# Performance work log

Hardware: AMD Instinct MI355X
Metric: run time of the kernel (lower is better)

The kernel has to match this reference:

```python
import jax, jax.numpy as jnp
import numpy as np

N_EMBED = 8192
EMBED_DIM = 32
BETA = 0.25
EPS_NORM = 1e-12   # torch F.normalize eps
EPS_ENT = 1e-4     # get_entropy eps


def _l2norm(x):
    n = jnp.linalg.norm(x, axis=-1, keepdims=True)
    return x / jnp.maximum(n, EPS_NORM)


def setup_inputs() -> dict:
    key = jax.random.key(0)
    k1, k2 = jax.random.split(key)
    z = jax.random.normal(k1, (32, EMBED_DIM, 32, 32), dtype=jnp.float32)
    # embedding.weight.data.uniform_(-1/n_embed, 1/n_embed)
    embedding = jax.random.uniform(k2, (N_EMBED, EMBED_DIM), dtype=jnp.float32,
                                   minval=-1.0 / N_EMBED, maxval=1.0 / N_EMBED)
    return {"z": z, "embedding": embedding}


def reference(z, embedding):
    batch = z.shape[0]
    # bchw -> bhwc
    zt = jnp.transpose(z, (0, 2, 3, 1))
    # l2_norm branch: cosine distance via negative inner product
    zn = _l2norm(zt)
    z_flat = zn.reshape(-1, EMBED_DIM)            # [N, D], N = B*H*W
    ew = _l2norm(embedding)                       # [K, D]
    d = -jnp.matmul(z_flat, ew.T)                 # [N, K] distance matrix
    idx = jnp.argmin(jax.lax.stop_gradient(d), axis=1)  # [N]
    # codebook usage histogram + entropy
    cb_usage = jax.ops.segment_sum(jnp.ones_like(idx, dtype=jnp.float32), idx,
                                   num_segments=N_EMBED)
    probs = (cb_usage + EPS_ENT) / jnp.sum(cb_usage + EPS_ENT)
    cb_entropy = -jnp.sum(probs * jnp.log(probs))
    # gather + re-normalize (faithful to embedding lookup then F.normalize)
    z_q = _l2norm(embedding[idx]).reshape(zn.shape)
    sg = jax.lax.stop_gradient
    loss = (BETA * jnp.mean(jnp.sum((sg(z_q) - zn) ** 2, axis=-1))
            + jnp.mean(jnp.sum((z_q - sg(zn)) ** 2, axis=-1)))
    # straight-through estimator
    z_q_st = zn + sg(z_q - zn)
    z_q_out = jnp.transpose(z_q_st, (0, 3, 1, 2))  # bhwc -> bchw
    return z_q_out, loss, cb_entropy, idx.reshape(batch, -1)
```

## Files before the change

kernel.cpp:

```cpp
#include <hip/hip_runtime.h>
#include <math.h>

#define N_EMBED 8192
#define DIM 32
#define NQ 32768

#define QPB 512
#define NQG (NQ / QPB)
#define KSPL 16
#define KCHUNK (N_EMBED / KSPL)
#define TILE 128
#define NTILES (KCHUNK / TILE)
#define NPLANE 8
#define LSTRIDE 130

#define LOSS_OFF  1048576
#define ENT_OFF   1048577
#define IDX_OFF   1048578

typedef __attribute__((ext_vector_type(8))) _Float16 half8;
typedef __attribute__((ext_vector_type(4))) float floatx4;

__global__ __launch_bounds__(512, 4) void score_kernel(const float* __restrict__ z,
                                                       const float* __restrict__ e,
                                                       unsigned long long* __restrict__ keys16,
                                                       unsigned* __restrict__ usage,
                                                       float* __restrict__ loss_acc,
                                                       unsigned* __restrict__ done_ctr) {
    __shared__ half8 lds[2][NPLANE * LSTRIDE];

    const int t = threadIdx.x;

    if (blockIdx.x == 0) {
        for (int i = t; i < N_EMBED; i += 512) usage[i] = 0u;
        if (t == 0) { loss_acc[0] = 0.f; done_ctr[0] = 0u; }
    }

    const int lane = t & 63;
    const int w = t >> 6;
    const int quad = lane >> 4;
    const int lc = lane & 15;
    const int qg = blockIdx.x & (NQG - 1);
    const int kc = blockIdx.x >> 6;
    const int kbase = kc * KCHUNK;
    const int qbase = qg * QPB + w * 64;

    half8 ah[4], am[4];
#pragma unroll
    for (int qt = 0; qt < 4; ++qt) {
        int q = qbase + qt * 16 + lc;
        const float* zp = z + (q >> 10) * (DIM * 1024) + (q & 1023);
        float x[8];
        float ss = 0.f;
#pragma unroll
        for (int j = 0; j < 8; ++j) {
            x[j] = zp[(quad * 8 + j) * 1024];
            ss = fmaf(x[j], x[j], ss);
        }
        ss += __shfl_xor(ss, 16, 64);
        ss += __shfl_xor(ss, 32, 64);
        float inv = 1.f / fmaxf(sqrtf(ss), 1e-12f);
#pragma unroll
        for (int j = 0; j < 8; ++j) {
            float xx = x[j] * inv;
            _Float16 h = (_Float16)xx;
            _Float16 m = (_Float16)((xx - (float)h) * 4096.0f);
            ah[qt][j] = h; am[qt][j] = m;
        }
    }

    auto stage = [&](int bsel, int kt) {
        const int ci = t >> 2;
        const int part = t & 3;
        const int code = kbase + kt * TILE + ci;
        const float4* er = (const float4*)(e + code * DIM) + part * 2;
        float4 v0 = er[0], v1 = er[1];
        float x[8] = {v0.x, v0.y, v0.z, v0.w, v1.x, v1.y, v1.z, v1.w};
        float ss = 0.f;
#pragma unroll
        for (int j = 0; j < 8; ++j) ss = fmaf(x[j], x[j], ss);
        ss += __shfl_xor(ss, 1, 64);
        ss += __shfl_xor(ss, 2, 64);
        float inv = 1.f / fmaxf(sqrtf(ss), 1e-12f);
        half8 h8, m8;
#pragma unroll
        for (int j = 0; j < 8; ++j) {
            float xx = x[j] * inv;
            _Float16 h = (_Float16)xx;
            _Float16 m = (_Float16)((xx - (float)h) * 4096.0f);
            h8[j] = h; m8[j] = m;
        }
        lds[bsel][part * LSTRIDE + ci] = h8;
        lds[bsel][(4 + part) * LSTRIDE + ci] = m8;
    };

    float best[16];
    int bk[16];
#pragma unroll
    for (int i = 0; i < 16; ++i) { best[i] = -2.0f; bk[i] = 0; }

    const floatx4 z4 = {0.f, 0.f, 0.f, 0.f};

    stage(0, 0);
    __syncthreads();

    for (int kt = 0; kt < NTILES; ++kt) {
        if (kt + 1 < NTILES) stage((kt + 1) & 1, kt + 1);

        const half8* __restrict__ buf = lds[kt & 1];
#pragma unroll 2
        for (int ct = 0; ct < TILE / 16; ++ct) {
            half8 bh = buf[(0 * 4 + quad) * LSTRIDE + ct * 16 + lc];
            half8 bm = buf[(1 * 4 + quad) * LSTRIDE + ct * 16 + lc];
            const int kk = kbase + kt * TILE + ct * 16 + lc;
#pragma unroll
            for (int qt = 0; qt < 4; ++qt) {
                floatx4 a0 = __builtin_amdgcn_mfma_f32_16x16x32_f16(ah[qt], bh, z4, 0, 0, 0);
                floatx4 a1 = __builtin_amdgcn_mfma_f32_16x16x32_f16(ah[qt], bm, z4, 0, 0, 0);
                a1 = __builtin_amdgcn_mfma_f32_16x16x32_f16(am[qt], bh, a1, 0, 0, 0);
#pragma unroll
                for (int r = 0; r < 4; ++r) {
                    float d = fmaf(a1[r], 0x1p-12f, a0[r]);
                    if (d > best[qt * 4 + r]) { best[qt * 4 + r] = d; bk[qt * 4 + r] = kk; }
                }
            }
        }
        __syncthreads();
    }

#pragma unroll
    for (int i = 0; i < 16; ++i) {
        unsigned ub = __float_as_uint(best[i]);
        ub = (ub & 0x80000000u) ? ~ub : (ub | 0x80000000u);
        unsigned long long key = ((unsigned long long)ub << 32) | (unsigned)(~bk[i]);
#pragma unroll
        for (int msk = 1; msk <= 8; msk <<= 1) {
            unsigned long long o = __shfl_xor(key, msk, 64);
            key = (o > key) ? o : key;
        }
        if (lc == 0) {
            int qt = i >> 2, r = i & 3;
            int q = qbase + qt * 16 + quad * 4 + r;
            keys16[kc * NQ + q] = key;
        }
    }
}

__global__ __launch_bounds__(256) void finalize_kernel(const float* __restrict__ z,
                                                       const float* __restrict__ e,
                                                       const unsigned long long* __restrict__ keys16,
                                                       unsigned* __restrict__ usage,
                                                       float* __restrict__ loss_acc,
                                                       unsigned* __restrict__ done_ctr,
                                                       float* __restrict__ out) {
    int n = blockIdx.x * 256 + threadIdx.x;
    int b  = n >> 10;
    int hw = n & 1023;
    const float* zb = z + b * (DIM * 1024) + hw;

    float q[DIM];
    float ss = 0.f;
#pragma unroll
    for (int d = 0; d < DIM; ++d) {
        q[d] = zb[d * 1024];
        ss = fmaf(q[d], q[d], ss);
    }
    float inv = 1.f / fmaxf(sqrtf(ss), 1e-12f);
#pragma unroll
    for (int d = 0; d < DIM; ++d) q[d] *= inv;

    unsigned long long bestkey = 0ull;
#pragma unroll
    for (int c = 0; c < KSPL; ++c) {
        unsigned long long k16 = keys16[c * NQ + n];
        bestkey = (k16 > bestkey) ? k16 : bestkey;
    }
    int idx = (int)(~(unsigned)(bestkey & 0xFFFFFFFFull));

    atomicAdd(&usage[idx], 1u);

    float wv[DIM];
    float ss2 = 0.f;
    const float4* er = (const float4*)(e + idx * DIM);
#pragma unroll
    for (int d8 = 0; d8 < 8; ++d8) {
        float4 t4 = er[d8];
        wv[d8*4+0] = t4.x; wv[d8*4+1] = t4.y; wv[d8*4+2] = t4.z; wv[d8*4+3] = t4.w;
        ss2 += t4.x*t4.x + t4.y*t4.y + t4.z*t4.z + t4.w*t4.w;
    }
    float inv2 = 1.f / fmaxf(sqrtf(ss2), 1e-12f);

    float lsum = 0.f;
    float* outb = out + b * (DIM * 1024) + hw;
#pragma unroll
    for (int d = 0; d < DIM; ++d) {
        float zq = wv[d] * inv2;
        float diff = zq - q[d];
        lsum = fmaf(diff, diff, lsum);
        outb[d * 1024] = q[d] + (zq - q[d]);
    }
    out[IDX_OFF + n] = (float)idx;

#pragma unroll
    for (int off = 32; off > 0; off >>= 1)
        lsum += __shfl_down(lsum, off, 64);
    if ((threadIdx.x & 63) == 0)
        atomicAdd(loss_acc, lsum);

    __shared__ unsigned lastflag;
    __syncthreads();
    if (threadIdx.x == 0) {
        __threadfence();
        unsigned prev = __hip_atomic_fetch_add(done_ctr, 1u, __ATOMIC_ACQ_REL,
                                               __HIP_MEMORY_SCOPE_AGENT);
        lastflag = (prev == gridDim.x - 1) ? 1u : 0u;
    }
    __syncthreads();
    if (lastflag) {
        __shared__ double sm[256];
        int t = threadIdx.x;
        double local = 0.0;
        const float denom = 32768.8192f;
        for (int k = t; k < N_EMBED; k += 256) {
            unsigned c = __hip_atomic_load(&usage[k], __ATOMIC_RELAXED,
                                           __HIP_MEMORY_SCOPE_AGENT);
            float p = ((float)c + 1e-4f) / denom;
            local += (double)(-(p * logf(p)));
        }
        sm[t] = local;
        __syncthreads();
        for (int s = 128; s > 0; s >>= 1) {
            if (t < s) sm[t] += sm[t + s];
            __syncthreads();
        }
        if (t == 0) {
            float la = __hip_atomic_load(loss_acc, __ATOMIC_RELAXED,
                                         __HIP_MEMORY_SCOPE_AGENT);
            out[LOSS_OFF] = (float)(1.25 * (double)la / 32768.0);
            out[ENT_OFF]  = (float)sm[0];
        }
    }
}

extern "C" void kernel_launch(void* const* d_in, const int* in_sizes, int n_in,
                              void* d_out, int out_size, void* d_ws, size_t ws_size,
                              hipStream_t stream) {
    const float* z   = (const float*)d_in[0];
    const float* emb = (const float*)d_in[1];
    float* out = (float*)d_out;

    char* ws = (char*)d_ws;
    unsigned long long* keys16 = (unsigned long long*)ws;
    unsigned* usage            = (unsigned*)(ws + (4 << 20));
    float* loss_acc            = (float*)(ws + (4 << 20) + 32768);
    unsigned* done_ctr         = (unsigned*)(ws + (4 << 20) + 32768 + 4);

    score_kernel<<<NQG * KSPL, 512, 0, stream>>>(z, emb, keys16, usage,
                                                 loss_acc, done_ctr);
    finalize_kernel<<<NQ / 256, 256, 0, stream>>>(z, emb, keys16, usage,
                                                  loss_acc, done_ctr, out);
}
```

Baseline: 144.4 us.

## Precompute split-fp16 normalized codebook in prep kernel, load whole chunk to LDS

Adds a prep kernel that normalizes the codebook once and writes fp16 hi/lo split planes to workspace. The old scheme renormalized each code in all 64 query-group blocks. The score kernel now copies its entire 512-code chunk (64KB) into LDS up front and runs the MFMA loop with no per-tile barriers or double buffering. In exchange it adds a kernel launch and a full-chunk LDS footprint, which drops occupancy to 2 blocks per CU, and it drops the LDS padding stride, which may cause bank conflicts.

```diff
diff --git a/kernel.cpp b/kernel.cpp
--- a/kernel.cpp
+++ b/kernel.cpp
@@ -9,10 +9,7 @@
 #define NQG (NQ / QPB)
 #define KSPL 16
 #define KCHUNK (N_EMBED / KSPL)
-#define TILE 128
-#define NTILES (KCHUNK / TILE)
-#define NPLANE 8
-#define LSTRIDE 130
+#define NCT (KCHUNK / 16)
 
 #define LOSS_OFF  1048576
 #define ENT_OFF   1048577
@@ -21,21 +18,46 @@
 typedef __attribute__((ext_vector_type(8))) _Float16 half8;
 typedef __attribute__((ext_vector_type(4))) float floatx4;
 
-__global__ __launch_bounds__(512, 4) void score_kernel(const float* __restrict__ z,
-                                                       const float* __restrict__ e,
-                                                       unsigned long long* __restrict__ keys16,
-                                                       unsigned* __restrict__ usage,
-                                                       float* __restrict__ loss_acc,
-                                                       unsigned* __restrict__ done_ctr) {
-    __shared__ half8 lds[2][NPLANE * LSTRIDE];
+__global__ __launch_bounds__(256) void prep_kernel(const float* __restrict__ e,
+                                                   half8* __restrict__ esplit,
+                                                   unsigned* __restrict__ usage,
+                                                   float* __restrict__ loss_acc,
+                                                   unsigned* __restrict__ done_ctr) {
+    int k = blockIdx.x * 256 + threadIdx.x;
+    const float4* src = (const float4*)(e + k * DIM);
+    float v[DIM];
+    float ss = 0.f;
+#pragma unroll
+    for (int i = 0; i < 8; ++i) {
+        float4 t = src[i];
+        v[i*4+0] = t.x; v[i*4+1] = t.y; v[i*4+2] = t.z; v[i*4+3] = t.w;
+        ss += t.x*t.x + t.y*t.y + t.z*t.z + t.w*t.w;
+    }
+    float inv = 1.f / fmaxf(sqrtf(ss), 1e-12f);
+    usage[k] = 0u;
+    if (k == 0) { loss_acc[0] = 0.f; done_ctr[0] = 0u; }
+
+#pragma unroll
+    for (int part = 0; part < 4; ++part) {
+        half8 h8, m8;
+#pragma unroll
+        for (int j = 0; j < 8; ++j) {
+            float xx = v[part * 8 + j] * inv;
+            _Float16 h = (_Float16)xx;
+            _Float16 m = (_Float16)((xx - (float)h) * 4096.0f);
+            h8[j] = h; m8[j] = m;
+        }
+        esplit[(0 * 4 + part) * N_EMBED + k] = h8;
+        esplit[(1 * 4 + part) * N_EMBED + k] = m8;
+    }
+}
+
+__global__ __launch_bounds__(512, 2) void score_kernel(const float* __restrict__ z,
+                                                       const half8* __restrict__ esplit,
+                                                       unsigned long long* __restrict__ keys16) {
+    __shared__ half8 lds[8 * KCHUNK];
 
     const int t = threadIdx.x;
-
-    if (blockIdx.x == 0) {
-        for (int i = t; i < N_EMBED; i += 512) usage[i] = 0u;
-        if (t == 0) { loss_acc[0] = 0.f; done_ctr[0] = 0u; }
-    }
-
     const int lane = t & 63;
     const int w = t >> 6;
     const int quad = lane >> 4;
@@ -45,6 +67,13 @@
     const int kbase = kc * KCHUNK;
     const int qbase = qg * QPB + w * 64;
 
+#pragma unroll
+    for (int j = 0; j < 8; ++j) {
+        int c = t + j * 512;
+        int p = c >> 9, i = c & 511;
+        lds[p * KCHUNK + i] = esplit[p * N_EMBED + kbase + i];
+    }
+
     half8 ah[4], am[4];
 #pragma unroll
     for (int qt = 0; qt < 4; ++qt) {
@@ -69,31 +98,6 @@
         }
     }
 
-    auto stage = [&](int bsel, int kt) {
-        const int ci = t >> 2;
-        const int part = t & 3;
-        const int code = kbase + kt * TILE + ci;
-        const float4* er = (const float4*)(e + code * DIM) + part * 2;
-        float4 v0 = er[0], v1 = er[1];
-        float x[8] = {v0.x, v0.y, v0.z, v0.w, v1.x, v1.y, v1.z, v1.w};
-        float ss = 0.f;
-#pragma unroll
-        for (int j = 0; j < 8; ++j) ss = fmaf(x[j], x[j], ss);
-        ss += __shfl_xor(ss, 1, 64);
-        ss += __shfl_xor(ss, 2, 64);
-        float inv = 1.f / fmaxf(sqrtf(ss), 1e-12f);
-        half8 h8, m8;
-#pragma unroll
-        for (int j = 0; j < 8; ++j) {
-            float xx = x[j] * inv;
-            _Float16 h = (_Float16)xx;
-            _Float16 m = (_Float16)((xx - (float)h) * 4096.0f);
-            h8[j] = h; m8[j] = m;
-        }
-        lds[bsel][part * LSTRIDE + ci] = h8;
-        lds[bsel][(4 + part) * LSTRIDE + ci] = m8;
-    };
-
     float best[16];
     int bk[16];
 #pragma unroll
@@ -101,31 +105,24 @@
 
     const floatx4 z4 = {0.f, 0.f, 0.f, 0.f};
 
-    stage(0, 0);
     __syncthreads();
 
-    for (int kt = 0; kt < NTILES; ++kt) {
-        if (kt + 1 < NTILES) stage((kt + 1) & 1, kt + 1);
-
-        const half8* __restrict__ buf = lds[kt & 1];
-#pragma unroll 2
-        for (int ct = 0; ct < TILE / 16; ++ct) {
-            half8 bh = buf[(0 * 4 + quad) * LSTRIDE + ct * 16 + lc];
-            half8 bm = buf[(1 * 4 + quad) * LSTRIDE + ct * 16 + lc];
-            const int kk = kbase + kt * TILE + ct * 16 + lc;
-#pragma unroll
-            for (int qt = 0; qt < 4; ++qt) {
-                floatx4 a0 = __builtin_amdgcn_mfma_f32_16x16x32_f16(ah[qt], bh, z4, 0, 0, 0);
-                floatx4 a1 = __builtin_amdgcn_mfma_f32_16x16x32_f16(ah[qt], bm, z4, 0, 0, 0);
-                a1 = __builtin_amdgcn_mfma_f32_16x16x32_f16(am[qt], bh, a1, 0, 0, 0);
-#pragma unroll
-                for (int r = 0; r < 4; ++r) {
-                    float d = fmaf(a1[r], 0x1p-12f, a0[r]);
-                    if (d > best[qt * 4 + r]) { best[qt * 4 + r] = d; bk[qt * 4 + r] = kk; }
-                }
+#pragma unroll 4
+    for (int ct = 0; ct < NCT; ++ct) {
+        half8 bh = lds[(0 * 4 + quad) * KCHUNK + ct * 16 + lc];
+        half8 bm = lds[(1 * 4 + quad) * KCHUNK + ct * 16 + lc];
+        const int kk = kbase + ct * 16 + lc;
+#pragma unroll
+        for (int qt = 0; qt < 4; ++qt) {
+            floatx4 a0 = __builtin_amdgcn_mfma_f32_16x16x32_f16(ah[qt], bh, z4, 0, 0, 0);
+            floatx4 a1 = __builtin_amdgcn_mfma_f32_16x16x32_f16(ah[qt], bm, z4, 0, 0, 0);
+            a1 = __builtin_amdgcn_mfma_f32_16x16x32_f16(am[qt], bh, a1, 0, 0, 0);
+#pragma unroll
+            for (int r = 0; r < 4; ++r) {
+                float d = fmaf(a1[r], 0x1p-12f, a0[r]);
+                if (d > best[qt * 4 + r]) { best[qt * 4 + r] = d; bk[qt * 4 + r] = kk; }
             }
         }
-        __syncthreads();
     }
 
 #pragma unroll
@@ -250,13 +247,15 @@
     float* out = (float*)d_out;
 
     char* ws = (char*)d_ws;
-    unsigned long long* keys16 = (unsigned long long*)ws;
-    unsigned* usage            = (unsigned*)(ws + (4 << 20));
-    float* loss_acc            = (float*)(ws + (4 << 20) + 32768);
-    unsigned* done_ctr         = (unsigned*)(ws + (4 << 20) + 32768 + 4);
-
-    score_kernel<<<NQG * KSPL, 512, 0, stream>>>(z, emb, keys16, usage,
-                                                 loss_acc, done_ctr);
+    half8* esplit              = (half8*)ws;
+    unsigned long long* keys16 = (unsigned long long*)(ws + (1 << 20));
+    unsigned* usage            = (unsigned*)(ws + (5 << 20));
+    float* loss_acc            = (float*)(ws + (5 << 20) + 32768);
+    unsigned* done_ctr         = (unsigned*)(ws + (5 << 20) + 32768 + 4);
+
+    prep_kernel<<<N_EMBED / 256, 256, 0, stream>>>(emb, esplit, usage,
+                                                   loss_acc, done_ctr);
+    score_kernel<<<NQG * KSPL, 512, 0, stream>>>(z, esplit, keys16);
     finalize_kernel<<<NQ / 256, 256, 0, stream>>>(z, emb, keys16, usage,
                                                   loss_acc, done_ctr, out);
 }
```

Result: slower. 148.8 us (+3.0%).
